# Kernel optimization log

Measured on AMD Instinct MI355X. Metric: run time of the kernel, lower is better.

The kernel has to match this reference:

```python
import jax, jax.numpy as jnp
import numpy as np

BIG = 1000000.0
EPS = 1e-06
COST_CLASS, COST_BBOX, COST_GIOU = 1.0, 5.0, 2.0


def sanitize_boxes(boxes):
    # boxes: [..., 4] cxcywh
    boxes = jnp.nan_to_num(boxes, nan=0.0, posinf=1.0, neginf=0.0)
    cx, cy, w, h = jnp.moveaxis(boxes, -1, 0)
    cx = jnp.clip(cx, 0.0, 1.0)
    cy = jnp.clip(cy, 0.0, 1.0)
    w = jnp.clip(w, EPS, 1.0)
    h = jnp.clip(h, EPS, 1.0)
    return jnp.stack([cx, cy, w, h], axis=-1)


def box_cxcywh_to_xyxy(x):
    cx, cy, w, h = jnp.moveaxis(x, -1, 0)
    return jnp.stack([cx - 0.5 * w, cy - 0.5 * h, cx + 0.5 * w, cy + 0.5 * h], axis=-1)


def pairwise_giou(b1, b2):
    # b1: [B, Q, 4] xyxy, b2: [B, T, 4] xyxy -> [B, Q, T]
    area1 = (b1[..., 2] - b1[..., 0]) * (b1[..., 3] - b1[..., 1])  # [B,Q]
    area2 = (b2[..., 2] - b2[..., 0]) * (b2[..., 3] - b2[..., 1])  # [B,T]
    lt = jnp.maximum(b1[:, :, None, :2], b2[:, None, :, :2])  # [B,Q,T,2]
    rb = jnp.minimum(b1[:, :, None, 2:], b2[:, None, :, 2:])
    wh = jnp.clip(rb - lt, 0.0)
    inter = wh[..., 0] * wh[..., 1]  # [B,Q,T]
    union = area1[:, :, None] + area2[:, None, :] - inter
    iou = inter / union
    # enclosing box
    lt_c = jnp.minimum(b1[:, :, None, :2], b2[:, None, :, :2])
    rb_c = jnp.maximum(b1[:, :, None, 2:], b2[:, None, :, 2:])
    wh_c = jnp.clip(rb_c - lt_c, 0.0)
    area_c = wh_c[..., 0] * wh_c[..., 1]
    return iou - (area_c - union) / area_c


def reference(pred_logits, pred_boxes, tgt_labels, tgt_boxes):
    # Batched cost-matrix construction of HungarianMatcher.forward.
    out_logits = jnp.nan_to_num(pred_logits, nan=0.0, posinf=0.0, neginf=0.0)
    out_prob = jax.nn.softmax(out_logits, axis=-1)  # [B,Q,C]
    out_bbox = sanitize_boxes(pred_boxes)           # [B,Q,4]
    t_bbox = sanitize_boxes(tgt_boxes)              # [B,T,4]

    # cost_class[b,q,t] = -out_prob[b,q,tgt_labels[b,t]]
    B, Q, C = out_prob.shape
    T = tgt_labels.shape[1]
    gather_idx = jnp.broadcast_to(tgt_labels[:, None, :], (B, Q, T))
    cost_class = -jnp.take_along_axis(out_prob, gather_idx, axis=2)  # [B,Q,T]

    # L1 cdist in cxcywh space
    cost_bbox = jnp.sum(jnp.abs(out_bbox[:, :, None, :] - t_bbox[:, None, :, :]), axis=-1)

    cost_giou = -pairwise_giou(box_cxcywh_to_xyxy(out_bbox), box_cxcywh_to_xyxy(t_bbox))

    Cmat = COST_CLASS * cost_class + COST_BBOX * cost_bbox + COST_GIOU * cost_giou
    return jnp.nan_to_num(Cmat, nan=BIG, posinf=BIG, neginf=BIG)


def setup_inputs() -> dict:
    key = jax.random.key(0)
    k1, k2, k3, k4 = jax.random.split(key, 4)
    B, Q, C, T = 64, 900, 256, 200
    return {
        "pred_logits": jax.random.normal(k1, (B, Q, C), dtype=jnp.float32),
        "pred_boxes": jax.random.uniform(k2, (B, Q, 4), dtype=jnp.float32),
        "tgt_labels": jax.random.randint(k3, (B, T), 0, C),
        "tgt_boxes": jax.random.uniform(k4, (B, T, 4), dtype=jnp.float32),
    }
```

## Files before the change

### kernel.cpp

```cpp
#include <hip/hip_runtime.h>
#include <math.h>

constexpr int B = 64, Q = 900, C = 256, T = 200;
constexpr float EPSV = 1e-6f;
constexpr int WPB = 4;
constexpr int QPW = 2;
constexpr int QPB = WPB * QPW;
constexpr int NT4 = T / 4;

__device__ __forceinline__ float clampf(float x, float lo, float hi) {
    return fminf(fmaxf(x, lo), hi);
}

__global__ __launch_bounds__(256, 6)
void matcher_kernel(const float* __restrict__ logits,
                    const float* __restrict__ pboxes,
                    const int*   __restrict__ tlabels,
                    const float* __restrict__ tboxes,
                    float* __restrict__ out)
{
    __shared__ float s_exp[WPB][C];

    const int blocks_per_b = (Q + QPB - 1) / QPB;
    const int b    = blockIdx.x / blocks_per_b;
    const int qblk = blockIdx.x % blocks_per_b;
    const int wave = threadIdx.x >> 6;
    const int lane = threadIdx.x & 63;
    const int q0   = qblk * QPB + wave * QPW;
    if (q0 >= Q) return;

    const bool act = lane < NT4;
    float tx0[4], ty0[4], tx1[4], ty1[4], twd[4], tht[4];
    int   lidx[4];
    {
        const float* tb_base = tboxes + b * (T * 4);
        const int*   tl_base = tlabels + b * T;
        const int t0i = act ? 4 * lane : 0;
        #pragma unroll
        for (int s = 0; s < 4; ++s) {
            int t = t0i + s;
            float4 tb = ((const float4*)tb_base)[t];
            float cx = clampf(tb.x, 0.0f, 1.0f);
            float cy = clampf(tb.y, 0.0f, 1.0f);
            float w  = clampf(tb.z, EPSV, 1.0f);
            float h  = clampf(tb.w, EPSV, 1.0f);
            twd[s] = w;  tht[s] = h;
            tx0[s] = cx - 0.5f * w;  ty0[s] = cy - 0.5f * h;
            tx1[s] = cx + 0.5f * w;  ty1[s] = cy + 0.5f * h;
            int lab = tl_base[t];
            lidx[s] = min(max(lab, 0), C - 1);
        }
    }

    #pragma unroll
    for (int i = 0; i < QPW; ++i) {
        const int q = q0 + i;
        if (q >= Q) break;
        const size_t row = (size_t)b * Q + q;

        const float4 lg = ((const float4*)(logits + row * C))[lane];
        const float4 pb = *(const float4*)(pboxes + row * 4);

        float e0 = __expf(lg.x), e1 = __expf(lg.y);
        float e2 = __expf(lg.z), e3 = __expf(lg.w);
        float ssum = (e0 + e1) + (e2 + e3);
        #pragma unroll
        for (int off = 32; off; off >>= 1) ssum += __shfl_xor(ssum, off);
        const float inv = __builtin_amdgcn_rcpf(ssum);

        ((float4*)&s_exp[wave][0])[lane] = make_float4(e0, e1, e2, e3);

        float pcx = clampf(pb.x, 0.0f, 1.0f), pcy = clampf(pb.y, 0.0f, 1.0f);
        float pw  = clampf(pb.z, EPSV, 1.0f), ph  = clampf(pb.w, EPSV, 1.0f);
        float px0 = pcx - 0.5f * pw, py0 = pcy - 0.5f * ph;
        float px1 = pcx + 0.5f * pw, py1 = pcy + 0.5f * ph;
        float psx = px0 + px1, psy = py0 + py1;
        float parea = pw * ph;

        float res[4];
        #pragma unroll
        for (int s = 0; s < 4; ++s) {
            float g  = s_exp[wave][lidx[s]];
            float t0 = fmaf(-g, inv, 2.0f);

            float s1 = fabsf(psx - (tx0[s] + tx1[s])) + fabsf(psy - (ty0[s] + ty1[s]));
            float s2 = fabsf(pw - twd[s]) + fabsf(ph - tht[s]);

            float iw = fmaxf(fminf(px1, tx1[s]) - fmaxf(px0, tx0[s]), 0.0f);
            float ih = fmaxf(fminf(py1, ty1[s]) - fmaxf(py0, ty0[s]), 0.0f);
            float inter = iw * ih;
            float uni = fmaf(twd[s], tht[s], parea) - inter;

            float cw = fmaxf(px1, tx1[s]) - fminf(px0, tx0[s]);
            float ch = fmaxf(py1, ty1[s]) - fminf(py0, ty0[s]);
            float ca = cw * ch;

            float num = fmaf(uni, uni, inter * ca);
            float val = num * __builtin_amdgcn_rcpf(uni * ca);

            float cost = fmaf(2.5f, s1, t0);
            cost = fmaf(5.0f, s2, cost);
            res[s] = fmaf(-2.0f, val, cost);
        }

        if (act) {
            float4* orow4 = (float4*)(out + row * T);
            orow4[lane] = make_float4(res[0], res[1], res[2], res[3]);
        }
    }
}

extern "C" void kernel_launch(void* const* d_in, const int* in_sizes, int n_in,
                              void* d_out, int out_size, void* d_ws, size_t ws_size,
                              hipStream_t stream) {
    const float* logits  = (const float*)d_in[0];
    const float* pboxes  = (const float*)d_in[1];
    const int*   tlabels = (const int*)d_in[2];
    const float* tboxes  = (const float*)d_in[3];
    float* out = (float*)d_out;

    const int blocks_per_b = (Q + QPB - 1) / QPB;
    dim3 grid(B * blocks_per_b);
    dim3 block(64 * WPB);
    matcher_kernel<<<grid, block, 0, stream>>>(logits, pboxes, tlabels, tboxes, out);
}
```

Baseline: 115.2 us.

## Use one query per wave, DPP softmax reduction, and vectorized target loads

Each wave now handles a single query row instead of two, which doubles the grid, and launch bounds are raised to allow more resident blocks. Logit and box loads are issued at the top of the kernel, and target labels are read as one int4. The wave-wide sum for the softmax now uses DPP row shifts and row broadcasts followed by a readlane, in place of shuffle-xor steps. The aim is more memory-level parallelism and cheaper reductions, at the cost of recomputing the per-target setup for every query.

```diff
diff --git a/kernel.cpp b/kernel.cpp
--- a/kernel.cpp
+++ b/kernel.cpp
@@ -4,15 +4,18 @@
 constexpr int B = 64, Q = 900, C = 256, T = 200;
 constexpr float EPSV = 1e-6f;
 constexpr int WPB = 4;
-constexpr int QPW = 2;
-constexpr int QPB = WPB * QPW;
+constexpr int QPB = WPB;
 constexpr int NT4 = T / 4;
 
 __device__ __forceinline__ float clampf(float x, float lo, float hi) {
     return fminf(fmaxf(x, lo), hi);
 }
 
-__global__ __launch_bounds__(256, 6)
+#define DPP_ADD_STEP(x, ctrl, row_mask)                                        \
+    (x) += __int_as_float(__builtin_amdgcn_update_dpp(                         \
+        0, __float_as_int(x), (ctrl), (row_mask), 0xf, true))
+
+__global__ __launch_bounds__(256, 8)
 void matcher_kernel(const float* __restrict__ logits,
                     const float* __restrict__ pboxes,
                     const int*   __restrict__ tlabels,
@@ -21,92 +24,95 @@
 {
     __shared__ float s_exp[WPB][C];
 
-    const int blocks_per_b = (Q + QPB - 1) / QPB;
+    const int blocks_per_b = Q / QPB;
     const int b    = blockIdx.x / blocks_per_b;
     const int qblk = blockIdx.x % blocks_per_b;
     const int wave = threadIdx.x >> 6;
     const int lane = threadIdx.x & 63;
-    const int q0   = qblk * QPB + wave * QPW;
-    if (q0 >= Q) return;
+    const int q    = qblk * QPB + wave;
+    const size_t row = (size_t)b * Q + q;
+
+    const float4 lg = ((const float4*)(logits + row * C))[lane];
+    const float4 pb = *(const float4*)(pboxes + row * 4);
 
     const bool act = lane < NT4;
+    const int  t0i = act ? 4 * lane : 0;
+    const float4* tb_base = (const float4*)(tboxes + b * (T * 4));
+    const float4 tb0 = tb_base[t0i + 0];
+    const float4 tb1 = tb_base[t0i + 1];
+    const float4 tb2 = tb_base[t0i + 2];
+    const float4 tb3 = tb_base[t0i + 3];
+    const int4 labs = *(const int4*)(tlabels + b * T + t0i);
+
     float tx0[4], ty0[4], tx1[4], ty1[4], twd[4], tht[4];
     int   lidx[4];
     {
-        const float* tb_base = tboxes + b * (T * 4);
-        const int*   tl_base = tlabels + b * T;
-        const int t0i = act ? 4 * lane : 0;
+        const float4 tbs[4] = {tb0, tb1, tb2, tb3};
+        const int    lbs[4] = {labs.x, labs.y, labs.z, labs.w};
         #pragma unroll
         for (int s = 0; s < 4; ++s) {
-            int t = t0i + s;
-            float4 tb = ((const float4*)tb_base)[t];
-            float cx = clampf(tb.x, 0.0f, 1.0f);
-            float cy = clampf(tb.y, 0.0f, 1.0f);
-            float w  = clampf(tb.z, EPSV, 1.0f);
-            float h  = clampf(tb.w, EPSV, 1.0f);
+            float cx = clampf(tbs[s].x, 0.0f, 1.0f);
+            float cy = clampf(tbs[s].y, 0.0f, 1.0f);
+            float w  = clampf(tbs[s].z, EPSV, 1.0f);
+            float h  = clampf(tbs[s].w, EPSV, 1.0f);
             twd[s] = w;  tht[s] = h;
             tx0[s] = cx - 0.5f * w;  ty0[s] = cy - 0.5f * h;
             tx1[s] = cx + 0.5f * w;  ty1[s] = cy + 0.5f * h;
-            int lab = tl_base[t];
-            lidx[s] = min(max(lab, 0), C - 1);
+            lidx[s] = min(max(lbs[s], 0), C - 1);
         }
     }
 
+    float e0 = __expf(lg.x), e1 = __expf(lg.y);
+    float e2 = __expf(lg.z), e3 = __expf(lg.w);
+    float ssum = (e0 + e1) + (e2 + e3);
+    DPP_ADD_STEP(ssum, 0x111, 0xf);
+    DPP_ADD_STEP(ssum, 0x112, 0xf);
+    DPP_ADD_STEP(ssum, 0x114, 0xf);
+    DPP_ADD_STEP(ssum, 0x118, 0xf);
+    DPP_ADD_STEP(ssum, 0x142, 0xa);
+    DPP_ADD_STEP(ssum, 0x143, 0xc);
+    const float total = __int_as_float(
+        __builtin_amdgcn_readlane(__float_as_int(ssum), 63));
+    const float inv = __builtin_amdgcn_rcpf(total);
+
+    ((float4*)&s_exp[wave][0])[lane] = make_float4(e0, e1, e2, e3);
+
+    float pcx = clampf(pb.x, 0.0f, 1.0f), pcy = clampf(pb.y, 0.0f, 1.0f);
+    float pw  = clampf(pb.z, EPSV, 1.0f), ph  = clampf(pb.w, EPSV, 1.0f);
+    float px0 = pcx - 0.5f * pw, py0 = pcy - 0.5f * ph;
+    float px1 = pcx + 0.5f * pw, py1 = pcy + 0.5f * ph;
+    float psx = px0 + px1, psy = py0 + py1;
+    float parea = pw * ph;
+
+    float res[4];
     #pragma unroll
-    for (int i = 0; i < QPW; ++i) {
-        const int q = q0 + i;
-        if (q >= Q) break;
-        const size_t row = (size_t)b * Q + q;
+    for (int s = 0; s < 4; ++s) {
+        float g  = s_exp[wave][lidx[s]];
+        float t0 = fmaf(-g, inv, 2.0f);
 
-        const float4 lg = ((const float4*)(logits + row * C))[lane];
-        const float4 pb = *(const float4*)(pboxes + row * 4);
+        float s1 = fabsf(psx - (tx0[s] + tx1[s])) + fabsf(psy - (ty0[s] + ty1[s]));
+        float s2 = fabsf(pw - twd[s]) + fabsf(ph - tht[s]);
 
-        float e0 = __expf(lg.x), e1 = __expf(lg.y);
-        float e2 = __expf(lg.z), e3 = __expf(lg.w);
-        float ssum = (e0 + e1) + (e2 + e3);
-        #pragma unroll
-        for (int off = 32; off; off >>= 1) ssum += __shfl_xor(ssum, off);
-        const float inv = __builtin_amdgcn_rcpf(ssum);
+        float iw = fmaxf(fminf(px1, tx1[s]) - fmaxf(px0, tx0[s]), 0.0f);
+        float ih = fmaxf(fminf(py1, ty1[s]) - fmaxf(py0, ty0[s]), 0.0f);
+        float inter = iw * ih;
+        float uni = fmaf(twd[s], tht[s], parea) - inter;
 
-        ((float4*)&s_exp[wave][0])[lane] = make_float4(e0, e1, e2, e3);
+        float cw = fmaxf(px1, tx1[s]) - fminf(px0, tx0[s]);
+        float ch = fmaxf(py1, ty1[s]) - fminf(py0, ty0[s]);
+        float ca = cw * ch;
 
-        float pcx = clampf(pb.x, 0.0f, 1.0f), pcy = clampf(pb.y, 0.0f, 1.0f);
-        float pw  = clampf(pb.z, EPSV, 1.0f), ph  = clampf(pb.w, EPSV, 1.0f);
-        float px0 = pcx - 0.5f * pw, py0 = pcy - 0.5f * ph;
-        float px1 = pcx + 0.5f * pw, py1 = pcy + 0.5f * ph;
-        float psx = px0 + px1, psy = py0 + py1;
-        float parea = pw * ph;
+        float num = fmaf(uni, uni, inter * ca);
+        float val = num * __builtin_amdgcn_rcpf(uni * ca);
 
-        float res[4];
-        #pragma unroll
-        for (int s = 0; s < 4; ++s) {
-            float g  = s_exp[wave][lidx[s]];
-            float t0 = fmaf(-g, inv, 2.0f);
+        float cost = fmaf(2.5f, s1, t0);
+        cost = fmaf(5.0f, s2, cost);
+        res[s] = fmaf(-2.0f, val, cost);
+    }
 
-            float s1 = fabsf(psx - (tx0[s] + tx1[s])) + fabsf(psy - (ty0[s] + ty1[s]));
-            float s2 = fabsf(pw - twd[s]) + fabsf(ph - tht[s]);
-
-            float iw = fmaxf(fminf(px1, tx1[s]) - fmaxf(px0, tx0[s]), 0.0f);
-            float ih = fmaxf(fminf(py1, ty1[s]) - fmaxf(py0, ty0[s]), 0.0f);
-            float inter = iw * ih;
-            float uni = fmaf(twd[s], tht[s], parea) - inter;
-
-            float cw = fmaxf(px1, tx1[s]) - fminf(px0, tx0[s]);
-            float ch = fmaxf(py1, ty1[s]) - fminf(py0, ty0[s]);
-            float ca = cw * ch;
-
-            float num = fmaf(uni, uni, inter * ca);
-            float val = num * __builtin_amdgcn_rcpf(uni * ca);
-
-            float cost = fmaf(2.5f, s1, t0);
-            cost = fmaf(5.0f, s2, cost);
-            res[s] = fmaf(-2.0f, val, cost);
-        }
-
-        if (act) {
-            float4* orow4 = (float4*)(out + row * T);
-            orow4[lane] = make_float4(res[0], res[1], res[2], res[3]);
-        }
+    if (act) {
+        float4* orow4 = (float4*)(out + row * T);
+        orow4[lane] = make_float4(res[0], res[1], res[2], res[3]);
     }
 }
 
@@ -119,8 +125,7 @@
     const float* tboxes  = (const float*)d_in[3];
     float* out = (float*)d_out;
 
-    const int blocks_per_b = (Q + QPB - 1) / QPB;
-    dim3 grid(B * blocks_per_b);
+    dim3 grid(B * (Q / QPB));
     dim3 block(64 * WPB);
     matcher_kernel<<<grid, block, 0, stream>>>(logits, pboxes, tlabels, tboxes, out);
 }
```

Measured after the change: 116.3 us. About the same (+0.9%).
